# Kernel tuning notes

Measured on AMD Instinct MI355X. Metric: run time of the kernel, lower is better.

Reference implementation:

```python
import jax, jax.numpy as jnp
import numpy as np

BIG = 1e9
EPS_BETA = 1e-6
EPS_BN = 1e-5

N_NODES = 50000
N_EDGES = 800000
IN_DIM = 128
OUT_DIM = 128


def setup_inputs() -> dict:
    key = jax.random.key(0)
    ks = jax.random.split(key, 8)
    h = jax.random.normal(ks[0], (N_NODES, IN_DIM), dtype=jnp.float32)
    src = jax.random.randint(ks[1], (N_EDGES,), 0, N_NODES, dtype=jnp.int32)
    dst = jax.random.randint(ks[2], (N_EDGES,), 0, N_NODES, dtype=jnp.int32)
    sigma_GD = jax.random.uniform(ks[3], (N_EDGES,), dtype=jnp.float32)
    fc_w = jax.random.normal(ks[4], (IN_DIM, OUT_DIM), dtype=jnp.float32) / np.sqrt(IN_DIM)
    fc_b = jax.random.normal(ks[5], (OUT_DIM,), dtype=jnp.float32) * 0.01
    attn_w = jax.random.normal(ks[6], (2 * OUT_DIM, 1), dtype=jnp.float32) / np.sqrt(2 * OUT_DIM)
    attn_b = jax.random.normal(ks[7], (1,), dtype=jnp.float32) * 0.01
    bn_gamma = jnp.ones((OUT_DIM,), dtype=jnp.float32)
    bn_beta = jnp.zeros((OUT_DIM,), dtype=jnp.float32)
    return {"h": h, "src": src, "dst": dst, "sigma_GD": sigma_GD,
            "fc_w": fc_w, "fc_b": fc_b, "attn_w": attn_w, "attn_b": attn_b,
            "bn_gamma": bn_gamma, "bn_beta": bn_beta}


def reference(h, src, dst, sigma_GD, fc_w, fc_b, attn_w, attn_b, bn_gamma, bn_beta):
    n = h.shape[0]
    # node projection
    z = h @ fc_w + fc_b                                   # [N, D]
    z = jnp.where(jnp.isinf(z), BIG, z)
    # per-edge attention logits: concat(src,dst) @ W == src@W1 + dst@W2 (avoid concat materialization)
    d = z.shape[1]
    w_src, w_dst = attn_w[:d], attn_w[d:]
    z_src = z[src]                                        # [E, D]
    a = z_src @ w_src + z[dst] @ w_dst + attn_b           # [E, 1]
    a = jnp.where(jnp.isinf(a), BIG, a)
    e = jax.nn.leaky_relu(a, negative_slope=0.01)[:, 0]   # [E]
    # segment softmax over incoming edges (mailbox softmax)
    m = jax.ops.segment_max(e, dst, num_segments=n)       # [N]
    ex = jnp.exp(e - m[dst])
    denom = jax.ops.segment_sum(ex, dst, num_segments=n)  # [N]
    alpha = ex / denom[dst]                               # [E]
    # beta: sigma_GD normalized per destination node
    bsum = jax.ops.segment_sum(sigma_GD, dst, num_segments=n)
    beta = sigma_GD / (bsum[dst] + EPS_BETA)              # [E]
    # weighted scatter-sum of source features
    h_new = jax.ops.segment_sum((alpha * beta)[:, None] * z_src, dst, num_segments=n)  # [N, D]
    h_new = jnp.where(jnp.isinf(h_new), BIG, h_new)
    # BatchNorm1d (training-mode batch stats, biased variance, as torch does)
    mu = h_new.mean(axis=0)
    var = ((h_new - mu) ** 2).mean(axis=0)
    h_bn = (h_new - mu) * jax.lax.rsqrt(var + EPS_BN) * bn_gamma + bn_beta
    return jax.nn.elu(h_bn)
```

## Files before the change

### kernel.cpp

```cpp
#include <hip/hip_runtime.h>
#include <hip/hip_fp16.h>
#include <math.h>

#define N_NODES 50000
#define N_EDGES 800000
#define BIGV 1000000000.0f
#define NBLK_GEMM 3125
#define CHUNK 4096
#define NCHUNK 196
#define NBUCKET 782
#define NB4 784

typedef _Float16 half8 __attribute__((ext_vector_type(8)));
typedef float floatx4 __attribute__((ext_vector_type(4)));

__device__ __forceinline__ float clampinf(float x) { return isinf(x) ? BIGV : x; }

__device__ __forceinline__ void barrier_lgkm_only() {
    __builtin_amdgcn_sched_barrier(0);
    asm volatile("s_waitcnt lgkmcnt(0)" ::: "memory");
    __builtin_amdgcn_s_barrier();
    __builtin_amdgcn_sched_barrier(0);
}

__global__ __launch_bounds__(256) void k_prep(const float* __restrict__ W,
                                              __half* __restrict__ wt,
                                              float* __restrict__ bns,
                                              const int* __restrict__ dst,
                                              int* __restrict__ counts)
{
    __shared__ int hist[NB4];
    const int t = threadIdx.x;
    const int idx = blockIdx.x * 256 + t;
    if (idx < 16384) {
        int n = idx >> 7, k = idx & 127;
        wt[idx] = __float2half(W[k * 128 + n]);
    }
    if (idx < 256) bns[idx] = 0.f;
    for (int i = t; i < NB4; i += 256) hist[i] = 0;
    __syncthreads();
    const int base = blockIdx.x * CHUNK;
    for (int i = t; i < CHUNK; i += 256) {
        int e = base + i;
        if (e < N_EDGES) atomicAdd(&hist[dst[e] >> 6], 1);
    }
    __syncthreads();
    for (int i = t; i < NB4; i += 256) counts[blockIdx.x * NB4 + i] = hist[i];
}

__global__ __launch_bounds__(256) void k_gemm(
    const float* __restrict__ h, const __half* __restrict__ wt,
    const float* __restrict__ bias, const float* __restrict__ attn_w,
    __half* __restrict__ zh, float* __restrict__ sv, float* __restrict__ tv)
{
    __shared__ _Float16 hA[16][136];
    __shared__ float spart[4][16], tpart[4][16];

    const int tid = threadIdx.x;
    const int lane = tid & 63;
    const int wv = tid >> 6;
    const int l16 = lane & 15;
    const int oct = lane >> 4;
    const int n0 = wv << 5;
    const int node0 = blockIdx.x << 4;

    {
        const float4* h4 = (const float4*)(h + (size_t)node0 * 128);
        for (int i = tid; i < 512; i += 256) {
            int r = i >> 5, c4 = i & 31;
            float4 v = h4[i];
            union { __half2 h2[2]; uint2 u; } pk;
            pk.h2[0] = __floats2half2_rn(v.x, v.y);
            pk.h2[1] = __floats2half2_rn(v.z, v.w);
            *(uint2*)&hA[r][c4 << 2] = pk.u;
        }
    }

    half8 bfrag[4][2];
    #pragma unroll
    for (int kk = 0; kk < 4; ++kk)
        #pragma unroll
        for (int t = 0; t < 2; ++t)
            bfrag[kk][t] = *(const half8*)(wt + (size_t)(n0 + t * 16 + l16) * 128
                                              + kk * 32 + oct * 8);

    const float bv0 = bias[n0 + l16],         bv1 = bias[n0 + 16 + l16];
    const float ws0 = attn_w[n0 + l16],       ws1 = attn_w[n0 + 16 + l16];
    const float wd0 = attn_w[128 + n0 + l16], wd1 = attn_w[128 + n0 + 16 + l16];

    barrier_lgkm_only();

    floatx4 acc0 = {0.f, 0.f, 0.f, 0.f};
    floatx4 acc1 = {0.f, 0.f, 0.f, 0.f};
    #pragma unroll
    for (int kk = 0; kk < 4; ++kk) {
        half8 a = *(const half8*)&hA[l16][(kk << 5) + (oct << 3)];
        acc0 = __builtin_amdgcn_mfma_f32_16x16x32_f16(a, bfrag[kk][0], acc0, 0, 0, 0);
        acc1 = __builtin_amdgcn_mfma_f32_16x16x32_f16(a, bfrag[kk][1], acc1, 0, 0, 0);
    }

    float s_acc[4], t_acc[4];
    #pragma unroll
    for (int r = 0; r < 4; ++r) {
        float z0 = clampinf(acc0[r] + bv0);
        float z1 = clampinf(acc1[r] + bv1);
        const int row = (oct << 2) + r;
        zh[(size_t)(node0 + row) * 128 + n0 + l16]      = __float2half(z0);
        zh[(size_t)(node0 + row) * 128 + n0 + 16 + l16] = __float2half(z1);
        s_acc[r] = z0 * ws0 + z1 * ws1;
        t_acc[r] = z0 * wd0 + z1 * wd1;
    }
    #pragma unroll
    for (int r = 0; r < 4; ++r) {
        #pragma unroll
        for (int o = 1; o < 16; o <<= 1) {
            s_acc[r] += __shfl_xor(s_acc[r], o);
            t_acc[r] += __shfl_xor(t_acc[r], o);
        }
    }
    if (l16 == 0) {
        #pragma unroll
        for (int r = 0; r < 4; ++r) {
            spart[wv][(oct << 2) + r] = s_acc[r];
            tpart[wv][(oct << 2) + r] = t_acc[r];
        }
    }
    barrier_lgkm_only();
    if (tid < 16) {
        sv[node0 + tid] = spart[0][tid] + spart[1][tid] + spart[2][tid] + spart[3][tid];
        tv[node0 + tid] = tpart[0][tid] + tpart[1][tid] + tpart[2][tid] + tpart[3][tid];
    }
}

__global__ __launch_bounds__(256) void k_scat(
    const int* __restrict__ src, const int* __restrict__ dst,
    const float* __restrict__ sigma,
    const float* __restrict__ sv, const float* __restrict__ tv,
    const float* __restrict__ attn_b, const int* __restrict__ counts,
    float4* __restrict__ tmp, int* __restrict__ bbase_g)
{
    __shared__ int cur[NB4];
    __shared__ int tsc[256];
    const int t = threadIdx.x;
    const int self = blockIdx.x;

    uint4 pre = {0u, 0u, 0u, 0u}, tot = {0u, 0u, 0u, 0u};
    if (t < 196) {
        const uint4* c4 = (const uint4*)counts;
        for (int c = 0; c < NCHUNK; ++c) {
            uint4 v = c4[c * (NB4 / 4) + t];
            tot.x += v.x; tot.y += v.y; tot.z += v.z; tot.w += v.w;
            if (c < self) { pre.x += v.x; pre.y += v.y; pre.z += v.z; pre.w += v.w; }
        }
    }
    const int tsum = (t < 196) ? (int)(tot.x + tot.y + tot.z + tot.w) : 0;
    tsc[t] = tsum;
    __syncthreads();
    for (int off = 1; off < 256; off <<= 1) {
        int u = (t >= off) ? tsc[t - off] : 0;
        __syncthreads();
        tsc[t] += u;
        __syncthreads();
    }
    if (t < 196) {
        const int v0 = tsc[t] - tsum;
        const int v1 = v0 + (int)tot.x;
        const int v2 = v1 + (int)tot.y;
        const int v3 = v2 + (int)tot.z;
        cur[4*t+0] = v0 + (int)pre.x;
        cur[4*t+1] = v1 + (int)pre.y;
        cur[4*t+2] = v2 + (int)pre.z;
        cur[4*t+3] = v3 + (int)pre.w;
        if (self == 0) {
            bbase_g[4*t+0] = v0; bbase_g[4*t+1] = v1;
            bbase_g[4*t+2] = v2; bbase_g[4*t+3] = v3;
        }
    }
    if (self == 0 && t == 0) bbase_g[NBUCKET] = N_EDGES;
    __syncthreads();

    const float ab = attn_b[0];
    const int base = self * CHUNK;
    for (int i = t; i < CHUNK; i += 256) {
        int e = base + i;
        if (e < N_EDGES) {
            int s = src[e];
            int d = dst[e];
            float a = sv[s] + tv[d] + ab;
            a = clampinf(a);
            float ev = a > 0.f ? a : 0.01f * a;
            int pos = atomicAdd(&cur[d >> 6], 1);
            float4 rec;
            rec.x = __int_as_float(s);
            rec.y = sigma[e];
            rec.z = ev;
            rec.w = __int_as_float(d);
            tmp[pos] = rec;
        }
    }
}

__global__ __launch_bounds__(256) void k_binB(const float4* __restrict__ tmp,
                                              const int* __restrict__ bbase_g,
                                              int* __restrict__ colptr,
                                              float4* __restrict__ recs)
{
    __shared__ int hist[64];
    __shared__ int cur[64];
    const int t = threadIdx.x;
    const int b = blockIdx.x;
    const int s0 = bbase_g[b];
    const int n = bbase_g[b + 1] - s0;
    if (t < 64) hist[t] = 0;
    __syncthreads();
    const float* tw = (const float*)tmp;
    for (int i = t; i < n; i += 256) {
        int d = __float_as_int(tw[4 * (size_t)(s0 + i) + 3]);
        atomicAdd(&hist[d & 63], 1);
    }
    __syncthreads();
    if (t < 64) {
        const int hv = hist[t];
        int x = hv;
        #pragma unroll
        for (int o = 1; o < 64; o <<= 1) {
            int u = __shfl_up(x, o);
            if (t >= o) x += u;
        }
        const int excl = x - hv;
        cur[t] = s0 + excl;
        const int node = (b << 6) + t;
        if (node < N_NODES) colptr[node] = s0 + excl;
    }
    if (b == 0 && t == 0) colptr[N_NODES] = N_EDGES;
    __syncthreads();
    for (int i = t; i < n; i += 256) {
        float4 rec = tmp[s0 + i];
        int d = __float_as_int(rec.w);
        int pos = atomicAdd(&cur[d & 63], 1);
        rec.w = 0.f;
        recs[pos] = rec;
    }
}

__global__ __launch_bounds__(256) void k_agg(
    const int* __restrict__ colptr, const float4* __restrict__ recs,
    const __half* __restrict__ zh, float* __restrict__ out)
{
    const int lane = threadIdx.x & 63;
    const int node = blockIdx.x * 4 + (threadIdx.x >> 6);
    if (node >= N_NODES) return;
    const int base = colptr[node];
    const int deg = colptr[node + 1] - base;

    const int grp = lane >> 4;
    const int l16 = lane & 15;
    float acc[8] = {0.f, 0.f, 0.f, 0.f, 0.f, 0.f, 0.f, 0.f};

    if (deg > 0) {
        if (deg <= 64) {
            int sidx = 0; float sig = 0.f, e = -INFINITY;
            if (lane < deg) {
                float4 r = recs[base + lane];
                sidx = __float_as_int(r.x); sig = r.y; e = r.z;
            }
            float m = e;
            for (int o = 32; o; o >>= 1) m = fmaxf(m, __shfl_xor(m, o));
            float p = (lane < deg) ? __expf(e - m) : 0.f;
            float dn = p, bs = sig;
            for (int o = 32; o; o >>= 1) {
                dn += __shfl_xor(dn, o);
                bs += __shfl_xor(bs, o);
            }
            const float coef = p * sig * (1.0f / dn) / (bs + 1e-6f);
            for (int c = 0; c < deg; c += 4) {
                const int j = c + grp;
                const int js = (j < deg) ? j : 0;
                float cf = __shfl(coef, js);
                int sj = __shfl(sidx, js);
                if (j < deg) {
                    uint4 raw = *(const uint4*)(zh + ((size_t)sj << 7) + (l16 << 3));
                    const __half2* hp = (const __half2*)&raw;
                    #pragma unroll
                    for (int k = 0; k < 4; ++k) {
                        float2 f = __half22float2(hp[k]);
                        acc[2*k]   = fmaf(cf, f.x, acc[2*k]);
                        acc[2*k+1] = fmaf(cf, f.y, acc[2*k+1]);
                    }
                }
            }
        } else {
            float m = -INFINITY;
            for (int i = lane; i < deg; i += 64) m = fmaxf(m, recs[base + i].z);
            for (int o = 32; o; o >>= 1) m = fmaxf(m, __shfl_xor(m, o));
            float dn = 0.f, bs = 0.f;
            for (int i = lane; i < deg; i += 64) {
                float4 r = recs[base + i];
                dn += __expf(r.z - m); bs += r.y;
            }
            for (int o = 32; o; o >>= 1) {
                dn += __shfl_xor(dn, o);
                bs += __shfl_xor(bs, o);
            }
            const float scale = (1.0f / dn) / (bs + 1e-6f);
            for (int c = 0; c < deg; c += 64) {
                int i = c + lane;
                int sidx = 0; float coef = 0.f;
                if (i < deg) {
                    float4 r = recs[base + i];
                    sidx = __float_as_int(r.x);
                    coef = __expf(r.z - m) * r.y * scale;
                }
                const int cnt2 = min(64, deg - c);
                for (int j = 0; j < cnt2; j += 4) {
                    const int jj = j + grp;
                    const int js = (jj < cnt2) ? jj : 0;
                    float cf = __shfl(coef, js);
                    int sj = __shfl(sidx, js);
                    if (jj < cnt2) {
                        uint4 raw = *(const uint4*)(zh + ((size_t)sj << 7) + (l16 << 3));
                        const __half2* hp = (const __half2*)&raw;
                        #pragma unroll
                        for (int k = 0; k < 4; ++k) {
                            float2 f = __half22float2(hp[k]);
                            acc[2*k]   = fmaf(cf, f.x, acc[2*k]);
                            acc[2*k+1] = fmaf(cf, f.y, acc[2*k+1]);
                        }
                    }
                }
            }
        }
    }
    #pragma unroll
    for (int k = 0; k < 8; ++k) {
        acc[k] += __shfl_xor(acc[k], 16);
        acc[k] += __shfl_xor(acc[k], 32);
    }
    if (grp == 0) {
        float4 o0, o1;
        o0.x = clampinf(acc[0]); o0.y = clampinf(acc[1]);
        o0.z = clampinf(acc[2]); o0.w = clampinf(acc[3]);
        o1.x = clampinf(acc[4]); o1.y = clampinf(acc[5]);
        o1.z = clampinf(acc[6]); o1.w = clampinf(acc[7]);
        float4* op = (float4*)(out + (size_t)node * 128 + (l16 << 3));
        op[0] = o0; op[1] = o1;
    }
}

__global__ __launch_bounds__(256) void k_bnstats(const float* __restrict__ hnew,
                                                 float* __restrict__ sums)
{
    const int tid = threadIdx.x;
    const int f4 = (tid & 31) << 2;
    const int rgrp = tid >> 5;
    float4 s = {0.f, 0.f, 0.f, 0.f}, q = {0.f, 0.f, 0.f, 0.f};
    for (int node = blockIdx.x * 8 + rgrp; node < N_NODES; node += 256 * 8) {
        float4 v = *(const float4*)(hnew + (size_t)node * 128 + f4);
        s.x += v.x; s.y += v.y; s.z += v.z; s.w += v.w;
        q.x += v.x * v.x; q.y += v.y * v.y; q.z += v.z * v.z; q.w += v.w * v.w;
    }
    __shared__ float4 ls[256], lq[256];
    ls[tid] = s; lq[tid] = q;
    __syncthreads();
    for (int off = 128; off >= 32; off >>= 1) {
        if (tid < off) {
            float4 a = ls[tid + off], b = lq[tid + off];
            ls[tid].x += a.x; ls[tid].y += a.y; ls[tid].z += a.z; ls[tid].w += a.w;
            lq[tid].x += b.x; lq[tid].y += b.y; lq[tid].z += b.z; lq[tid].w += b.w;
        }
        __syncthreads();
    }
    if (tid < 32) {
        float4 fs = ls[tid], fq = lq[tid];
        atomicAdd(&sums[f4 + 0], fs.x);
        atomicAdd(&sums[f4 + 1], fs.y);
        atomicAdd(&sums[f4 + 2], fs.z);
        atomicAdd(&sums[f4 + 3], fs.w);
        atomicAdd(&sums[128 + f4 + 0], fq.x);
        atomicAdd(&sums[128 + f4 + 1], fq.y);
        atomicAdd(&sums[128 + f4 + 2], fq.z);
        atomicAdd(&sums[128 + f4 + 3], fq.w);
    }
}

__global__ __launch_bounds__(256) void k_bnapply(float* __restrict__ io,
                                                 const float* __restrict__ sums,
                                                 const float* __restrict__ gamma,
                                                 const float* __restrict__ beta)
{
    __shared__ float sc[128], sh[128];
    const int tid = threadIdx.x;
    if (tid < 128) {
        const float invn = 1.0f / (float)N_NODES;
        float mu = sums[tid] * invn;
        float var = fmaxf(sums[128 + tid] * invn - mu * mu, 0.f);
        float g = gamma[tid] * rsqrtf(var + 1e-5f);
        sc[tid] = g;
        sh[tid] = beta[tid] - mu * g;
    }
    __syncthreads();
    const size_t idx = (size_t)blockIdx.x * 256 + tid;
    const int f4 = ((int)idx & 31) << 2;
    float4 x = ((const float4*)io)[idx];
    float y0 = x.x * sc[f4 + 0] + sh[f4 + 0];
    float y1 = x.y * sc[f4 + 1] + sh[f4 + 1];
    float y2 = x.z * sc[f4 + 2] + sh[f4 + 2];
    float y3 = x.w * sc[f4 + 3] + sh[f4 + 3];
    float4 o;
    o.x = y0 > 0.f ? y0 : expm1f(y0);
    o.y = y1 > 0.f ? y1 : expm1f(y1);
    o.z = y2 > 0.f ? y2 : expm1f(y2);
    o.w = y3 > 0.f ? y3 : expm1f(y3);
    ((float4*)io)[idx] = o;
}

extern "C" void kernel_launch(void* const* d_in, const int* in_sizes, int n_in,
                              void* d_out, int out_size, void* d_ws, size_t ws_size,
                              hipStream_t stream)
{
    const float* h      = (const float*)d_in[0];
    const int*   src    = (const int*)  d_in[1];
    const int*   dst    = (const int*)  d_in[2];
    const float* sigma  = (const float*)d_in[3];
    const float* fc_w   = (const float*)d_in[4];
    const float* fc_b   = (const float*)d_in[5];
    const float* attn_w = (const float*)d_in[6];
    const float* attn_b = (const float*)d_in[7];
    const float* gamma  = (const float*)d_in[8];
    const float* beta   = (const float*)d_in[9];
    float* out = (float*)d_out;

    float4* recs   = (float4*)d_ws;
    float4* tmp    = recs + N_EDGES;
    __half* zh     = (__half*)(tmp + N_EDGES);
    float*  sv     = (float*)(zh + (size_t)N_NODES * 128);
    float*  tv     = sv + N_NODES;
    float*  bns    = tv + N_NODES;
    int*    colptr = (int*)(bns + 256);
    __half* wt     = (__half*)(colptr + 50004);
    int*    counts = (int*)(wt + 16384);
    int*    bbase  = counts + NCHUNK * NB4;

    k_prep    <<<NCHUNK, 256, 0, stream>>>(fc_w, wt, bns, dst, counts);
    k_gemm    <<<NBLK_GEMM, 256, 0, stream>>>(h, wt, fc_b, attn_w, zh, sv, tv);
    k_scat    <<<NCHUNK, 256, 0, stream>>>(src, dst, sigma, sv, tv, attn_b,
                                           counts, tmp, bbase);
    k_binB    <<<NBUCKET, 256, 0, stream>>>(tmp, bbase, colptr, recs);
    k_agg     <<<N_NODES / 4, 256, 0, stream>>>(colptr, recs, zh, out);
    k_bnstats <<<256, 256, 0, stream>>>(out, bns);
    k_bnapply <<<(N_NODES * 128) / (256 * 4), 256, 0, stream>>>(out, bns, gamma, beta);
}
```

Measured before the change: 235.5 us.

## Add dedicated per-bucket scan kernel and shrink scatter chunks for more parallelism

Edge chunks for histogramming and scattering shrink, so more blocks are launched for the two edge passes. Chunk counts are stored transposed, and a new k_off kernel does one wavefront-level prefix scan per bucket to produce per-chunk cursors and bucket totals. k_scat no longer makes every block re-sum the full counts matrix serially; each block just loads its own cursor row and scans the bucket totals. This removes redundant O(NCHUNK) work per block in exchange for an extra launch and larger count/cursor arrays.

```diff
diff --git a/kernel.cpp b/kernel.cpp
--- a/kernel.cpp
+++ b/kernel.cpp
@@ -6,8 +6,8 @@
 #define N_EDGES 800000
 #define BIGV 1000000000.0f
 #define NBLK_GEMM 3125
-#define CHUNK 4096
-#define NCHUNK 196
+#define CHUNK 1024
+#define NCHUNK 782
 #define NBUCKET 782
 #define NB4 784
 
@@ -27,7 +27,7 @@
                                               __half* __restrict__ wt,
                                               float* __restrict__ bns,
                                               const int* __restrict__ dst,
-                                              int* __restrict__ counts)
+                                              int* __restrict__ countsT)
 {
     __shared__ int hist[NB4];
     const int t = threadIdx.x;
@@ -45,7 +45,36 @@
         if (e < N_EDGES) atomicAdd(&hist[dst[e] >> 6], 1);
     }
     __syncthreads();
-    for (int i = t; i < NB4; i += 256) counts[blockIdx.x * NB4 + i] = hist[i];
+    for (int i = t; i < NB4; i += 256)
+        countsT[i * NB4 + blockIdx.x] = hist[i];
+}
+
+__global__ __launch_bounds__(256) void k_off(const int* __restrict__ countsT,
+                                             int* __restrict__ cursC,
+                                             int* __restrict__ btot)
+{
+    const int wv = (blockIdx.x << 2) + (threadIdx.x >> 6);
+    const int l = threadIdx.x & 63;
+    if (wv >= NBUCKET) {
+        if (l == 0 && wv < NB4) btot[wv] = 0;
+        return;
+    }
+    const int* row = countsT + (size_t)wv * NB4;
+    int carry = 0;
+    #pragma unroll
+    for (int p = 0; p < 13; ++p) {
+        const int c = p * 64 + l;
+        const int v = (c < NCHUNK) ? row[c] : 0;
+        int x = v;
+        #pragma unroll
+        for (int o = 1; o < 64; o <<= 1) {
+            int u = __shfl_up(x, o);
+            if (l >= o) x += u;
+        }
+        if (c < NCHUNK) cursC[(size_t)c * NB4 + wv] = carry + x - v;
+        carry += __shfl(x, 63);
+    }
+    if (l == 0) btot[wv] = carry;
 }
 
 __global__ __launch_bounds__(256) void k_gemm(
@@ -136,24 +165,24 @@
     const int* __restrict__ src, const int* __restrict__ dst,
     const float* __restrict__ sigma,
     const float* __restrict__ sv, const float* __restrict__ tv,
-    const float* __restrict__ attn_b, const int* __restrict__ counts,
+    const float* __restrict__ attn_b,
+    const int* __restrict__ cursC, const int* __restrict__ btot,
     float4* __restrict__ tmp, int* __restrict__ bbase_g)
 {
     __shared__ int cur[NB4];
+    __shared__ int bb[NB4];
     __shared__ int tsc[256];
     const int t = threadIdx.x;
     const int self = blockIdx.x;
 
-    uint4 pre = {0u, 0u, 0u, 0u}, tot = {0u, 0u, 0u, 0u};
+    for (int i = t; i < NB4; i += 256) cur[i] = cursC[(size_t)self * NB4 + i];
+
+    uint4 bt = {0u, 0u, 0u, 0u};
+    int tsum = 0;
     if (t < 196) {
-        const uint4* c4 = (const uint4*)counts;
-        for (int c = 0; c < NCHUNK; ++c) {
-            uint4 v = c4[c * (NB4 / 4) + t];
-            tot.x += v.x; tot.y += v.y; tot.z += v.z; tot.w += v.w;
-            if (c < self) { pre.x += v.x; pre.y += v.y; pre.z += v.z; pre.w += v.w; }
-        }
-    }
-    const int tsum = (t < 196) ? (int)(tot.x + tot.y + tot.z + tot.w) : 0;
+        bt = ((const uint4*)btot)[t];
+        tsum = (int)(bt.x + bt.y + bt.z + bt.w);
+    }
     tsc[t] = tsum;
     __syncthreads();
     for (int off = 1; off < 256; off <<= 1) {
@@ -164,19 +193,15 @@
     }
     if (t < 196) {
         const int v0 = tsc[t] - tsum;
-        const int v1 = v0 + (int)tot.x;
-        const int v2 = v1 + (int)tot.y;
-        const int v3 = v2 + (int)tot.z;
-        cur[4*t+0] = v0 + (int)pre.x;
-        cur[4*t+1] = v1 + (int)pre.y;
-        cur[4*t+2] = v2 + (int)pre.z;
-        cur[4*t+3] = v3 + (int)pre.w;
-        if (self == 0) {
-            bbase_g[4*t+0] = v0; bbase_g[4*t+1] = v1;
-            bbase_g[4*t+2] = v2; bbase_g[4*t+3] = v3;
-        }
-    }
-    if (self == 0 && t == 0) bbase_g[NBUCKET] = N_EDGES;
+        bb[4*t+0] = v0;
+        bb[4*t+1] = v0 + (int)bt.x;
+        bb[4*t+2] = v0 + (int)bt.x + (int)bt.y;
+        bb[4*t+3] = v0 + (int)bt.x + (int)bt.y + (int)bt.z;
+    }
+    __syncthreads();
+    for (int i = t; i < NB4; i += 256) cur[i] += bb[i];
+    if (self == 0)
+        for (int i = t; i < NB4; i += 256) bbase_g[i] = bb[i];
     __syncthreads();
 
     const float ab = attn_b[0];
@@ -210,7 +235,7 @@
     const int t = threadIdx.x;
     const int b = blockIdx.x;
     const int s0 = bbase_g[b];
-    const int n = bbase_g[b + 1] - s0;
+    const int n = ((b + 1 < NB4) ? bbase_g[b + 1] : N_EDGES) - s0;
     if (t < 64) hist[t] = 0;
     __syncthreads();
     const float* tw = (const float*)tmp;
@@ -438,13 +463,16 @@
     float*  bns    = tv + N_NODES;
     int*    colptr = (int*)(bns + 256);
     __half* wt     = (__half*)(colptr + 50004);
-    int*    counts = (int*)(wt + 16384);
-    int*    bbase  = counts + NCHUNK * NB4;
-
-    k_prep    <<<NCHUNK, 256, 0, stream>>>(fc_w, wt, bns, dst, counts);
+    int*    countsT= (int*)(wt + 16384);
+    int*    cursC  = countsT + NB4 * NB4;
+    int*    btot   = cursC + NB4 * NB4;
+    int*    bbase  = btot + NB4;
+
+    k_prep    <<<NCHUNK, 256, 0, stream>>>(fc_w, wt, bns, dst, countsT);
+    k_off     <<<196, 256, 0, stream>>>(countsT, cursC, btot);
     k_gemm    <<<NBLK_GEMM, 256, 0, stream>>>(h, wt, fc_b, attn_w, zh, sv, tv);
     k_scat    <<<NCHUNK, 256, 0, stream>>>(src, dst, sigma, sv, tv, attn_b,
-                                           counts, tmp, bbase);
+                                           cursC, btot, tmp, bbase);
     k_binB    <<<NBUCKET, 256, 0, stream>>>(tmp, bbase, colptr, recs);
     k_agg     <<<N_NODES / 4, 256, 0, stream>>>(colptr, recs, zh, out);
     k_bnstats <<<256, 256, 0, stream>>>(out, bns);
```

New measurement: 225.4 us. 4.3% less time.
